# Kernel tuning notes

Hardware: AMD Instinct MI355X
Metric: run time of the kernel (lower is better)

Reference implementation:

```python
import jax, jax.numpy as jnp
import numpy as np

D_MODEL = 2048
NUM_EXPERTS = 128
TOP_K = 8
NORM_P = 2.0  # normalize_expert_weights


def setup_inputs() -> dict:
    key = jax.random.key(0)
    k1, k2 = jax.random.split(key)
    x = jax.random.normal(k1, (4, 4096, D_MODEL), dtype=jnp.float32)
    # router weight ~ trunc_normal(std=0.02); plain normal*0.02 is fine for a numeric baseline
    weight = jax.random.normal(k2, (NUM_EXPERTS, D_MODEL), dtype=jnp.float32) * 0.02
    score_bias = jnp.zeros((NUM_EXPERTS,), dtype=jnp.float32)
    return {"x": x, "weight": weight, "score_bias": score_bias}


def reference(x, weight, score_bias):
    # Flatten tokens: (B, S, D) -> (N, D); router always runs in fp32 (x.float())
    B, S, D = x.shape
    xf = x.reshape(B * S, D).astype(jnp.float32)
    # get_expert_logits: F.linear(x, weight.view(E, D)) -> (N, E)
    logits = jnp.einsum("nd,ed->ne", xf, weight.astype(jnp.float32))
    # softmax gating
    scores = jax.nn.softmax(logits, axis=-1)
    # bias-adjusted top-k (bias only affects selection, not the returned weights)
    biased = scores + score_bias[None, :]
    _, expert_indices = jax.lax.top_k(biased, TOP_K)          # (N, top_k)
    expert_weights = jnp.take_along_axis(scores, expert_indices, axis=-1)
    # normalize_expert_weights = 2.0 -> divide by L2 norm across top_k
    norm = jnp.linalg.norm(expert_weights, ord=NORM_P, axis=-1, keepdims=True)
    expert_weights = expert_weights / norm
    return expert_weights, expert_indices
```

## Files before the change

kernel.cpp:

```cpp
#include <hip/hip_runtime.h>
#include <math.h>


#define NE      128
#define TOKT    64
#define KC      32
#define DMODEL  2048
#define NT      (DMODEL / KC)
#define CHUNK_SH (3 * NE * KC)
#define XPAD    40

typedef __attribute__((ext_vector_type(8))) short short8;
typedef __attribute__((ext_vector_type(4))) short s16x4;
typedef __attribute__((ext_vector_type(4))) float f32x4;

union S4u { short s[4]; s16x4 v; };

__device__ __forceinline__ void split3(float f, S4u& hi, S4u& mi, S4u& lo, int j) {
  const unsigned u0 = __float_as_uint(f);
  const float hif = __uint_as_float(u0 & 0xFFFF0000u);
  const float r1 = f - hif;
  const unsigned u1 = __float_as_uint(r1);
  const float mif = __uint_as_float(u1 & 0xFFFF0000u);
  const float r2 = r1 - mif;
  hi.s[j] = (short)(u0 >> 16);
  mi.s[j] = (short)(u1 >> 16);
  lo.s[j] = (short)(__float_as_uint(r2) >> 16);
}

__global__ __launch_bounds__(256) void wprep(const float* __restrict__ w,
                                             short* __restrict__ wp) {
  const int gid = blockIdx.x * 256 + threadIdx.x;
  const int e = gid >> 9;
  const int g = gid & 511;
  const int k = g << 2;
  const int chunk = k >> 5;
  const int kk = k & 31;
  const f32x4 a = *(const f32x4*)(w + (size_t)e * DMODEL + k);
  S4u hi, mi, lo;
  split3(a[0], hi, mi, lo, 0); split3(a[1], hi, mi, lo, 1);
  split3(a[2], hi, mi, lo, 2); split3(a[3], hi, mi, lo, 3);
  short* base = wp + (size_t)chunk * CHUNK_SH + (size_t)e * KC + kk;
  *(s16x4*)(base)               = hi.v;
  *(s16x4*)(base + NE * KC)     = mi.v;
  *(s16x4*)(base + 2 * NE * KC) = lo.v;
}

__global__ __launch_bounds__(512) void router_fused(
    const float* __restrict__ x, const short* __restrict__ wp,
    const float* __restrict__ bias, float* __restrict__ outW,
    float* __restrict__ outI, int N) {
  __shared__ __align__(16) char arena[TOKT * (NE + 2) * 4];
  typedef short XsmT[3][TOKT][XPAD];
  XsmT* xsm = (XsmT*)arena;
  float (*L)[NE + 2] = (float (*)[NE + 2])arena;

  const int tid  = threadIdx.x;
  const int wv   = tid >> 6;
  const int lane = tid & 63;
  const int wm   = wv >> 2;
  const int wn   = wv & 3;
  const int quad = lane >> 4;
  const int l16  = lane & 15;
  const size_t tokBase = (size_t)blockIdx.x * TOKT;

  const int r  = tid >> 3;
  const int kq = tid & 7;
  const float* xg = x + (tokBase + r) * (size_t)DMODEL + kq * 4;

  const short* wfb = wp + (size_t)(wn * 32 + l16) * KC + quad * 8;

  f32x4 accs[4][2][2];
#pragma unroll
  for (int s = 0; s < 4; ++s)
#pragma unroll
    for (int i = 0; i < 2; ++i)
#pragma unroll
      for (int j = 0; j < 2; ++j) accs[s][i][j] = (f32x4)(0.f);

  auto load_bf = [&](short8 (&bf)[2][3], int c) {
    const short* b = wfb + (size_t)c * CHUNK_SH;
#pragma unroll
    for (int nt = 0; nt < 2; ++nt)
#pragma unroll
      for (int p = 0; p < 3; ++p)
        bf[nt][p] = *(const short8*)(b + p * (NE * KC) + nt * 16 * KC);
  };
  auto stage_x = [&](int buf, f32x4 xr) {
    S4u hi, mi, lo;
    split3(xr[0], hi, mi, lo, 0); split3(xr[1], hi, mi, lo, 1);
    split3(xr[2], hi, mi, lo, 2); split3(xr[3], hi, mi, lo, 3);
    *(s16x4*)&xsm[buf][0][r][kq * 4] = hi.v;
    *(s16x4*)&xsm[buf][1][r][kq * 4] = mi.v;
    *(s16x4*)&xsm[buf][2][r][kq * 4] = lo.v;
  };
  auto compute = [&](int buf, const short8 (&bf)[2][3], f32x4 (&acc)[2][2]) {
    short8 af[2][3];
#pragma unroll
    for (int mt = 0; mt < 2; ++mt)
#pragma unroll
      for (int p = 0; p < 3; ++p)
        af[mt][p] = *(const short8*)&xsm[buf][p][wm * 32 + mt * 16 + l16][quad * 8];
#pragma unroll
    for (int nt = 0; nt < 2; ++nt)
#pragma unroll
      for (int mt = 0; mt < 2; ++mt) {
        f32x4 c = acc[mt][nt];
        c = __builtin_amdgcn_mfma_f32_16x16x32_bf16(af[mt][0], bf[nt][0], c, 0, 0, 0);
        c = __builtin_amdgcn_mfma_f32_16x16x32_bf16(af[mt][0], bf[nt][1], c, 0, 0, 0);
        c = __builtin_amdgcn_mfma_f32_16x16x32_bf16(af[mt][1], bf[nt][0], c, 0, 0, 0);
        c = __builtin_amdgcn_mfma_f32_16x16x32_bf16(af[mt][0], bf[nt][2], c, 0, 0, 0);
        c = __builtin_amdgcn_mfma_f32_16x16x32_bf16(af[mt][2], bf[nt][0], c, 0, 0, 0);
        c = __builtin_amdgcn_mfma_f32_16x16x32_bf16(af[mt][1], bf[nt][1], c, 0, 0, 0);
        acc[mt][nt] = c;
      }
  };
  auto lds_barrier = [&]() {
    asm volatile("s_waitcnt lgkmcnt(0)" ::: "memory");
    __builtin_amdgcn_s_barrier();
  };

  short8 bfA[2][3], bfB[2][3];
  load_bf(bfA, 0);
  f32x4 xra = *(const f32x4*)(xg);
  f32x4 xrb = *(const f32x4*)(xg + KC);
  stage_x(0, xra);
  lds_barrier();

#pragma unroll
  for (int s = 0; s < 4; ++s) {
#pragma unroll 1
    for (int u = 0; u < 16; u += 2) {
      const int t = s * 16 + u;
      if (t + 1 < NT) load_bf(bfB, t + 1);
      if (t + 2 < NT) xra = *(const f32x4*)(xg + (t + 2) * KC);
      compute(0, bfA, accs[s]);
      if (t + 1 < NT) { stage_x(1, xrb); lds_barrier(); }
      if (t + 2 < NT) load_bf(bfA, t + 2);
      if (t + 3 < NT) xrb = *(const f32x4*)(xg + (t + 3) * KC);
      if (t + 1 < NT) compute(1, bfB, accs[s]);
      if (t + 2 < NT) { stage_x(0, xra); lds_barrier(); }
    }
  }

  __syncthreads();

#pragma unroll
  for (int mt = 0; mt < 2; ++mt)
#pragma unroll
    for (int nt = 0; nt < 2; ++nt)
#pragma unroll
      for (int reg = 0; reg < 4; ++reg) {
        float v = accs[0][mt][nt][reg];
        v += accs[1][mt][nt][reg];
        v += accs[2][mt][nt][reg];
        v += accs[3][mt][nt][reg];
        L[wm * 32 + mt * 16 + quad * 4 + reg][wn * 32 + nt * 16 + l16] = v;
      }
  __syncthreads();

  const float bmy0 = bias[lane];
  const float bmy1 = bias[lane + 64];
  for (int i = 0; i < 8; ++i) {
    const int tk = wv * 8 + i;
    const float l0 = L[tk][lane];
    const float l1 = L[tk][lane + 64];

    float m = fmaxf(l0, l1);
#pragma unroll
    for (int off = 1; off < 64; off <<= 1) m = fmaxf(m, __shfl_xor(m, off));
    const float ev0 = __expf(l0 - m);
    const float ev1 = __expf(l1 - m);
    float zs = ev0 + ev1;
#pragma unroll
    for (int off = 1; off < 64; off <<= 1) zs += __shfl_xor(zs, off);
    const float s0 = ev0 / zs;
    const float s1 = ev1 / zs;

    float b0 = s0 + bmy0;
    float b1 = s1 + bmy1;

    float myv = 0.f;
    int myi = 0;
    float ss = 0.f;
#pragma unroll
    for (int rnd = 0; rnd < 8; ++rnd) {
      float key; int idx;
      if (b0 >= b1) { key = b0; idx = lane; }
      else          { key = b1; idx = lane + 64; }
#pragma unroll
      for (int off = 1; off < 64; off <<= 1) {
        const float k2 = __shfl_xor(key, off);
        const int   i2 = __shfl_xor(idx, off);
        if (k2 > key || (k2 == key && i2 < idx)) { key = k2; idx = i2; }
      }
      const float cand = (idx < 64) ? s0 : s1;
      const float sw = __shfl(cand, idx & 63);
      ss = fmaf(sw, sw, ss);
      if (lane == rnd) { myv = sw; myi = idx; }
      if (lane == (idx & 63)) { if (idx < 64) b0 = -INFINITY; else b1 = -INFINITY; }
    }

    const float inv = 1.f / sqrtf(ss);
    if (lane < 8) {
      const size_t tok = tokBase + tk;
      outW[tok * 8 + lane] = myv * inv;
      outI[tok * 8 + lane] = (float)myi;
    }
  }
}

extern "C" void kernel_launch(void* const* d_in, const int* in_sizes, int n_in,
                              void* d_out, int out_size, void* d_ws, size_t ws_size,
                              hipStream_t stream) {
  const float* x    = (const float*)d_in[0];
  const float* w    = (const float*)d_in[1];
  const float* bias = (const float*)d_in[2];
  float* out = (float*)d_out;

  const int N = in_sizes[0] / DMODEL;
  short* wp = (short*)d_ws;

  wprep<<<256, 256, 0, stream>>>(w, wp);
  router_fused<<<N / TOKT, 512, 0, stream>>>(x, wp, bias, out, out + (size_t)N * 8, N);
}
```

Before: 273.6 us.

## Halve token tile to 32 per block and raise occupancy hint

Cuts the per-block token tile from 64 to 32, so each wave computes a single 16-row M tile and each thread stages two x values instead of four. Doubles the grid size and adds a min-blocks-per-CU hint of 4 to launch bounds. The aim is lower register use and LDS footprint for higher occupancy and more blocks across CUs. In exchange, the split weight fragments are reloaded from global memory twice as often per token, and each MFMA has less operand reuse.

```diff
diff --git a/kernel.cpp b/kernel.cpp
--- a/kernel.cpp
+++ b/kernel.cpp
@@ -3,7 +3,7 @@
 
 
 #define NE      128
-#define TOKT    64
+#define TOKT    32
 #define KC      32
 #define DMODEL  2048
 #define NT      (DMODEL / KC)
@@ -13,6 +13,7 @@
 typedef __attribute__((ext_vector_type(8))) short short8;
 typedef __attribute__((ext_vector_type(4))) short s16x4;
 typedef __attribute__((ext_vector_type(4))) float f32x4;
+typedef __attribute__((ext_vector_type(2))) float f32x2;
 
 union S4u { short s[4]; s16x4 v; };
 
@@ -46,7 +47,7 @@
   *(s16x4*)(base + 2 * NE * KC) = lo.v;
 }
 
-__global__ __launch_bounds__(512) void router_fused(
+__global__ __launch_bounds__(512, 4) void router_fused(
     const float* __restrict__ x, const short* __restrict__ wp,
     const float* __restrict__ bias, float* __restrict__ outW,
     float* __restrict__ outI, int N) {
@@ -64,19 +65,17 @@
   const int l16  = lane & 15;
   const size_t tokBase = (size_t)blockIdx.x * TOKT;
 
-  const int r  = tid >> 3;
-  const int kq = tid & 7;
-  const float* xg = x + (tokBase + r) * (size_t)DMODEL + kq * 4;
+  const int r  = tid >> 4;
+  const int kp = (tid & 15) * 2;
+  const float* xg = x + (tokBase + r) * (size_t)DMODEL + kp;
 
   const short* wfb = wp + (size_t)(wn * 32 + l16) * KC + quad * 8;
 
-  f32x4 accs[4][2][2];
+  f32x4 accs[4][2];
 #pragma unroll
   for (int s = 0; s < 4; ++s)
 #pragma unroll
-    for (int i = 0; i < 2; ++i)
-#pragma unroll
-      for (int j = 0; j < 2; ++j) accs[s][i][j] = (f32x4)(0.f);
+    for (int j = 0; j < 2; ++j) accs[s][j] = (f32x4)(0.f);
 
   auto load_bf = [&](short8 (&bf)[2][3], int c) {
     const short* b = wfb + (size_t)c * CHUNK_SH;
@@ -86,34 +85,32 @@
       for (int p = 0; p < 3; ++p)
         bf[nt][p] = *(const short8*)(b + p * (NE * KC) + nt * 16 * KC);
   };
-  auto stage_x = [&](int buf, f32x4 xr) {
+  auto stage_x = [&](int buf, f32x2 xr) {
     S4u hi, mi, lo;
     split3(xr[0], hi, mi, lo, 0); split3(xr[1], hi, mi, lo, 1);
-    split3(xr[2], hi, mi, lo, 2); split3(xr[3], hi, mi, lo, 3);
-    *(s16x4*)&xsm[buf][0][r][kq * 4] = hi.v;
-    *(s16x4*)&xsm[buf][1][r][kq * 4] = mi.v;
-    *(s16x4*)&xsm[buf][2][r][kq * 4] = lo.v;
-  };
-  auto compute = [&](int buf, const short8 (&bf)[2][3], f32x4 (&acc)[2][2]) {
-    short8 af[2][3];
-#pragma unroll
-    for (int mt = 0; mt < 2; ++mt)
-#pragma unroll
-      for (int p = 0; p < 3; ++p)
-        af[mt][p] = *(const short8*)&xsm[buf][p][wm * 32 + mt * 16 + l16][quad * 8];
-#pragma unroll
-    for (int nt = 0; nt < 2; ++nt)
-#pragma unroll
-      for (int mt = 0; mt < 2; ++mt) {
-        f32x4 c = acc[mt][nt];
-        c = __builtin_amdgcn_mfma_f32_16x16x32_bf16(af[mt][0], bf[nt][0], c, 0, 0, 0);
-        c = __builtin_amdgcn_mfma_f32_16x16x32_bf16(af[mt][0], bf[nt][1], c, 0, 0, 0);
-        c = __builtin_amdgcn_mfma_f32_16x16x32_bf16(af[mt][1], bf[nt][0], c, 0, 0, 0);
-        c = __builtin_amdgcn_mfma_f32_16x16x32_bf16(af[mt][0], bf[nt][2], c, 0, 0, 0);
-        c = __builtin_amdgcn_mfma_f32_16x16x32_bf16(af[mt][2], bf[nt][0], c, 0, 0, 0);
-        c = __builtin_amdgcn_mfma_f32_16x16x32_bf16(af[mt][1], bf[nt][1], c, 0, 0, 0);
-        acc[mt][nt] = c;
-      }
+    *(int*)&xsm[buf][0][r][kp] =
+        (int)(unsigned short)hi.s[0] | ((int)(unsigned short)hi.s[1] << 16);
+    *(int*)&xsm[buf][1][r][kp] =
+        (int)(unsigned short)mi.s[0] | ((int)(unsigned short)mi.s[1] << 16);
+    *(int*)&xsm[buf][2][r][kp] =
+        (int)(unsigned short)lo.s[0] | ((int)(unsigned short)lo.s[1] << 16);
+  };
+  auto compute = [&](int buf, const short8 (&bf)[2][3], f32x4 (&acc)[2]) {
+    short8 af[3];
+#pragma unroll
+    for (int p = 0; p < 3; ++p)
+      af[p] = *(const short8*)&xsm[buf][p][wm * 16 + l16][quad * 8];
+#pragma unroll
+    for (int nt = 0; nt < 2; ++nt) {
+      f32x4 c = acc[nt];
+      c = __builtin_amdgcn_mfma_f32_16x16x32_bf16(af[0], bf[nt][0], c, 0, 0, 0);
+      c = __builtin_amdgcn_mfma_f32_16x16x32_bf16(af[0], bf[nt][1], c, 0, 0, 0);
+      c = __builtin_amdgcn_mfma_f32_16x16x32_bf16(af[1], bf[nt][0], c, 0, 0, 0);
+      c = __builtin_amdgcn_mfma_f32_16x16x32_bf16(af[0], bf[nt][2], c, 0, 0, 0);
+      c = __builtin_amdgcn_mfma_f32_16x16x32_bf16(af[2], bf[nt][0], c, 0, 0, 0);
+      c = __builtin_amdgcn_mfma_f32_16x16x32_bf16(af[1], bf[nt][1], c, 0, 0, 0);
+      acc[nt] = c;
+    }
   };
   auto lds_barrier = [&]() {
     asm volatile("s_waitcnt lgkmcnt(0)" ::: "memory");
@@ -122,8 +119,8 @@
 
   short8 bfA[2][3], bfB[2][3];
   load_bf(bfA, 0);
-  f32x4 xra = *(const f32x4*)(xg);
-  f32x4 xrb = *(const f32x4*)(xg + KC);
+  f32x2 xra = *(const f32x2*)(xg);
+  f32x2 xrb = *(const f32x2*)(xg + KC);
   stage_x(0, xra);
   lds_barrier();
 
@@ -133,11 +130,11 @@
     for (int u = 0; u < 16; u += 2) {
       const int t = s * 16 + u;
       if (t + 1 < NT) load_bf(bfB, t + 1);
-      if (t + 2 < NT) xra = *(const f32x4*)(xg + (t + 2) * KC);
+      if (t + 2 < NT) xra = *(const f32x2*)(xg + (t + 2) * KC);
       compute(0, bfA, accs[s]);
       if (t + 1 < NT) { stage_x(1, xrb); lds_barrier(); }
       if (t + 2 < NT) load_bf(bfA, t + 2);
-      if (t + 3 < NT) xrb = *(const f32x4*)(xg + (t + 3) * KC);
+      if (t + 3 < NT) xrb = *(const f32x2*)(xg + (t + 3) * KC);
       if (t + 1 < NT) compute(1, bfB, accs[s]);
       if (t + 2 < NT) { stage_x(0, xra); lds_barrier(); }
     }
@@ -146,23 +143,21 @@
   __syncthreads();
 
 #pragma unroll
-  for (int mt = 0; mt < 2; ++mt)
-#pragma unroll
-    for (int nt = 0; nt < 2; ++nt)
-#pragma unroll
-      for (int reg = 0; reg < 4; ++reg) {
-        float v = accs[0][mt][nt][reg];
-        v += accs[1][mt][nt][reg];
-        v += accs[2][mt][nt][reg];
-        v += accs[3][mt][nt][reg];
-        L[wm * 32 + mt * 16 + quad * 4 + reg][wn * 32 + nt * 16 + l16] = v;
-      }
+  for (int nt = 0; nt < 2; ++nt)
+#pragma unroll
+    for (int reg = 0; reg < 4; ++reg) {
+      float v = accs[0][nt][reg];
+      v += accs[1][nt][reg];
+      v += accs[2][nt][reg];
+      v += accs[3][nt][reg];
+      L[wm * 16 + quad * 4 + reg][wn * 32 + nt * 16 + l16] = v;
+    }
   __syncthreads();
 
   const float bmy0 = bias[lane];
   const float bmy1 = bias[lane + 64];
-  for (int i = 0; i < 8; ++i) {
-    const int tk = wv * 8 + i;
+  for (int i = 0; i < 4; ++i) {
+    const int tk = wv * 4 + i;
     const float l0 = L[tk][lane];
     const float l1 = L[tk][lane + 64];
 
```

Result: slower. 292.7 us (+7.0%).
